# Kernel optimization log

Hardware: AMD Instinct MI355X
Metric: run time of the kernel (lower is better)

## Reference

```python
import jax, jax.numpy as jnp
import numpy as np

N_NODES = 100000
N_EDGES = 1600000
DIM = 64


def setup_inputs() -> dict:
    key = jax.random.key(0)
    ks = jax.random.split(key, 10)
    return {
        "h_real": jax.random.normal(ks[0], (N_NODES, DIM), dtype=jnp.float32),
        "h_imag": jax.random.normal(ks[1], (N_NODES, DIM), dtype=jnp.float32),
        "d": jax.random.uniform(ks[2], (N_NODES,), dtype=jnp.float32),
        "w_real": jax.random.normal(ks[3], (N_EDGES,), dtype=jnp.float32),
        "w_imag": jax.random.normal(ks[4], (N_EDGES,), dtype=jnp.float32),
        "src": jax.random.randint(ks[5], (N_EDGES,), 0, N_NODES, dtype=jnp.int32),
        "dst": jax.random.randint(ks[6], (N_EDGES,), 0, N_NODES, dtype=jnp.int32),
        "W1": jax.random.normal(ks[7], (DIM, DIM), dtype=jnp.float32) * (1.414 / np.sqrt(DIM)),
        "b1": jnp.zeros((DIM,), dtype=jnp.float32),
        "W2": jax.random.normal(ks[8], (DIM, DIM), dtype=jnp.float32) * (1.414 / np.sqrt(DIM)),
        "b2": jnp.zeros((DIM,), dtype=jnp.float32),
    }


def reference(h_real, h_imag, d, w_real, w_imag, src, dst, W1, b1, W2, b2):
    n = h_real.shape[0]
    # per-edge complex coefficient e = d_dst * d_src * (w_real + i w_imag)
    dd = d[dst] * d[src]                      # [E]
    e_r = (dd * w_real)[:, None]              # [E,1]
    e_i = (dd * w_imag)[:, None]              # [E,1]
    hr = h_real[src]                          # [E,D]
    hi = h_imag[src]                          # [E,D]
    # complex multiply e * h, fused single pass over edges
    m_r = e_r * hr - e_i * hi                 # [E,D]
    m_i = e_i * hr + e_r * hi                 # [E,D]
    z_real = jax.ops.segment_sum(m_r, dst, num_segments=n)  # [N,D]
    z_imag = jax.ops.segment_sum(m_i, dst, num_segments=n)  # [N,D]
    # note: original overwrites z_real first, then z_imag uses the NEW z_real
    zr = (z_real @ W1.T + b1) - (z_imag @ W2.T + b2)
    zi = (zr @ W2.T + b2) + (z_imag @ W1.T + b1)
    return zr, zi
```

## Files before the change

kernel.cpp:

```cpp
#include <hip/hip_runtime.h>
#include <hip/hip_bf16.h>

#define N_NODES 100000
#define N_EDGES 1600000
#define DIM 64

#define TILE 4096
#define B1 ((N_EDGES + TILE - 1) / TILE)
#define K1 ((N_NODES + 255) / 256)
#define NCOUNTS (K1 * B1)
#define SCAN_BLOCK 1024
#define NSB ((NCOUNTS + SCAN_BLOCK - 1) / SCAN_BLOCK)
#define PACKB ((N_NODES * DIM + 255) / 256)
#define PLACE_CAP 4736

typedef __attribute__((ext_vector_type(8))) short bf16x8;
typedef __attribute__((ext_vector_type(4))) float f32x4;

#if defined(__has_builtin)
#if __has_builtin(__builtin_amdgcn_fdot2_f32_bf16)
#define HAVE_DOT2 1
typedef __attribute__((ext_vector_type(2))) __bf16 bf16x2v;
#endif
#endif


__device__ __forceinline__ unsigned pack_bf16x2(float lo, float hi) {
  unsigned ulo = (unsigned)__hip_bfloat16_raw(__float2bfloat16(lo)).x;
  unsigned uhi = (unsigned)__hip_bfloat16_raw(__float2bfloat16(hi)).x;
  return ulo | (uhi << 16);
}
__device__ __forceinline__ float unpack_lo(unsigned u) {
  return __int_as_float((int)(u << 16));
}
__device__ __forceinline__ float unpack_hi(unsigned u) {
  return __int_as_float((int)(u & 0xFFFF0000u));
}
__device__ __forceinline__ unsigned short f2bf(float x) {
  return __hip_bfloat16_raw(__float2bfloat16(x)).x;
}

__global__ __launch_bounds__(256) void setup_fused_kernel(
    const float* __restrict__ h_real, const float* __restrict__ h_imag,
    unsigned* __restrict__ hpack, const float* __restrict__ W1,
    const float* __restrict__ b1, const float* __restrict__ W2,
    const float* __restrict__ b2, unsigned short* __restrict__ At,
    float* __restrict__ cvec, const int* __restrict__ dst,
    int* __restrict__ counts) {
  const int bid = blockIdx.x;
  const int tid = threadIdx.x;
  if (bid < PACKB) {
    const int i = bid * 256 + tid;
    if (i < N_NODES * DIM) hpack[i] = pack_bf16x2(h_real[i], h_imag[i]);
    return;
  }
  if (bid < PACKB + 64) {
    const int idx = (bid - PACKB) * 256 + tid;
    if (idx < 128 * 128) {
      const int n = idx >> 7, k = idx & 127;
      float v;
      if (n < 64) {
        v = (k < 64) ? W1[n * 64 + k] : -W2[n * 64 + (k - 64)];
      } else {
        const int nn = n - 64;
        if (k < 64) {
          float s = 0.0f;
          for (int j = 0; j < 64; ++j) s += W1[j * 64 + k] * W2[nn * 64 + j];
          v = s;
        } else {
          const int kk = k - 64;
          float s = 0.0f;
          for (int j = 0; j < 64; ++j) s += W2[j * 64 + kk] * W2[nn * 64 + j];
          v = W1[nn * 64 + kk] - s;
        }
      }
      At[n * 128 + k] = f2bf(v);
    }
    if (idx < 128) {
      if (idx < 64) {
        cvec[idx] = b1[idx] - b2[idx];
      } else {
        const int nn = idx - 64;
        float s = 0.0f;
        for (int j = 0; j < 64; ++j) s += (b1[j] - b2[j]) * W2[nn * 64 + j];
        cvec[idx] = s + b1[nn] + b2[nn];
      }
    }
    return;
  }
  __shared__ int lh[K1];
  const int hb = bid - PACKB - 64;
  for (int i = tid; i < K1; i += 256) lh[i] = 0;
  __syncthreads();
  const int e0 = hb * TILE;
  const int e1 = min(e0 + TILE, N_EDGES);
  for (int e = e0 + tid; e < e1; e += 256) atomicAdd(&lh[dst[e] >> 8], 1);
  __syncthreads();
  for (int b = tid; b < K1; b += 256) counts[b * B1 + hb] = lh[b];
}

__global__ __launch_bounds__(SCAN_BLOCK) void scan1_kernel(
    int* __restrict__ cnt, int* __restrict__ bsum) {
  __shared__ int s[SCAN_BLOCK];
  const int tid = threadIdx.x;
  const int i = blockIdx.x * SCAN_BLOCK + tid;
  const int v = (i < NCOUNTS) ? cnt[i] : 0;
  s[tid] = v;
  __syncthreads();
#pragma unroll
  for (int off = 1; off < SCAN_BLOCK; off <<= 1) {
    int t = (tid >= off) ? s[tid - off] : 0;
    __syncthreads();
    s[tid] += t;
    __syncthreads();
  }
  if (i < NCOUNTS) cnt[i] = s[tid] - v;
  if (tid == SCAN_BLOCK - 1) bsum[blockIdx.x] = s[tid];
}

__global__ void scan2_kernel(const int* __restrict__ bsum, int* __restrict__ bpre) {
  if (threadIdx.x == 0 && blockIdx.x == 0) {
    int run = 0;
    for (int b = 0; b < NSB; ++b) {
      bpre[b] = run;
      run += bsum[b];
    }
  }
}

__global__ __launch_bounds__(SCAN_BLOCK) void scan3_kernel(
    int* __restrict__ cnt, const int* __restrict__ bpre) {
  const int i = blockIdx.x * SCAN_BLOCK + threadIdx.x;
  if (i < NCOUNTS) cnt[i] += bpre[blockIdx.x];
}

__global__ __launch_bounds__(512) void partition_kernel(
    const int* __restrict__ src, const int* __restrict__ dst,
    const float* __restrict__ dvec,
    const float* __restrict__ w_real, const float* __restrict__ w_imag,
    const int* __restrict__ coffs, unsigned long long* __restrict__ records) {
  __shared__ unsigned long long stage[TILE];
  __shared__ unsigned short sb[TILE];
  __shared__ int lhist[512];
  __shared__ int lbase[K1];
  __shared__ int lcur[K1];
  __shared__ int gbase[K1];
  const int tid = threadIdx.x;
  const int blk = blockIdx.x;
  const int e0 = blk * TILE;
  const int cnt_t = min(TILE, N_EDGES - e0);

  lhist[tid] = 0;
  __syncthreads();
  for (int j = tid; j < cnt_t; j += 512) atomicAdd(&lhist[dst[e0 + j] >> 8], 1);
  __syncthreads();
  const int myc = lhist[tid];
  __syncthreads();
#pragma unroll
  for (int off = 1; off < 512; off <<= 1) {
    int v = (tid >= off) ? lhist[tid - off] : 0;
    __syncthreads();
    lhist[tid] += v;
    __syncthreads();
  }
  if (tid < K1) {
    const int ex = lhist[tid] - myc;
    lbase[tid] = ex;
    lcur[tid] = ex;
    gbase[tid] = coffs[tid * B1 + blk];
  }
  __syncthreads();

  for (int j = tid; j < cnt_t; j += 512) {
    const int e = e0 + j;
    const int t = dst[e];
    const int s = src[e];
    const int b = t >> 8;
    const float ds = dvec[s];
    const unsigned lo = (unsigned)s | ((unsigned)(t & 255) << 17);
    const unsigned hi = pack_bf16x2(ds * w_real[e], ds * w_imag[e]);
    const int r = atomicAdd(&lcur[b], 1);
    stage[r] = ((unsigned long long)hi << 32) | lo;
    sb[r] = (unsigned short)b;
  }
  __syncthreads();
  for (int i = tid; i < cnt_t; i += 512) {
    const int b = sb[i];
    records[gbase[b] + (i - lbase[b])] = stage[i];
  }
}

__global__ __launch_bounds__(256) void place_kernel(
    unsigned long long* __restrict__ records, const int* __restrict__ coffs,
    int* __restrict__ inc) {
  const int b = blockIdx.x;
  const int tid = threadIdx.x;
  const int bstart = coffs[b * B1];
  const int bend = (b == K1 - 1) ? N_EDGES : coffs[(b + 1) * B1];
  const int cnt = min(bend - bstart, PLACE_CAP);
  const int nbase = b << 8;
  const int nn = min(256, N_NODES - nbase);

  __shared__ unsigned long long stage[PLACE_CAP];
  __shared__ int ncnt[256];
  __shared__ int ncur[256];

  ncnt[tid] = 0;
  __syncthreads();
  for (int i = tid; i < cnt; i += 256) {
    const unsigned long long rec = records[bstart + i];
    stage[i] = rec;
    atomicAdd(&ncnt[((unsigned)rec >> 17) & 255], 1);
  }
  __syncthreads();
  const int myc = ncnt[tid];
  __syncthreads();
#pragma unroll
  for (int off = 1; off < 256; off <<= 1) {
    int v = (tid >= off) ? ncnt[tid - off] : 0;
    __syncthreads();
    ncnt[tid] += v;
    __syncthreads();
  }
  const int base = bstart + ncnt[tid] - myc;
  ncur[tid] = base;
  if (tid < nn) inc[nbase + tid] = base + myc;
  __syncthreads();
  for (int i = tid; i < cnt; i += 256) {
    const unsigned long long rec = stage[i];
    const int pos = atomicAdd(&ncur[((unsigned)rec >> 17) & 255], 1);
    records[pos] = rec;
  }
}

__global__ __launch_bounds__(1024) void pull_fused_kernel(
    const uint2* __restrict__ records, const int* __restrict__ inc,
    const float* __restrict__ dvec, const unsigned* __restrict__ hpack,
    const unsigned short* __restrict__ At, const float* __restrict__ cvec,
    float* __restrict__ zr_out, float* __restrict__ zi_out) {
  __shared__ __align__(16) unsigned short zs[16][136];
  const int lane = threadIdx.x & 63;
  const int wave = threadIdx.x >> 6;
  const int q4 = lane >> 4;
  const int m16 = lane & 15;
  const int node0 = blockIdx.x * 16;
  const int n = node0 + wave;

  const int start = (n == 0) ? 0 : inc[n - 1];
  const int end = inc[n];
  const int deg = end - start;
  const unsigned* __restrict__ hb = hpack + 4 * m16;

  float sr0 = 0.f, sr1 = 0.f, sr2 = 0.f, sr3 = 0.f;
  float si0 = 0.f, si1 = 0.f, si2 = 0.f, si3 = 0.f;

#if HAVE_DOT2
#define DOT2(acc, w, h)                                                     \
  acc = __builtin_amdgcn_fdot2_f32_bf16(__builtin_bit_cast(bf16x2v, (w)),   \
                                        __builtin_bit_cast(bf16x2v, (h)),   \
                                        acc, false)
#else
#define DOT2(acc, w, h)                                                     \
  {                                                                         \
    const float _wl = unpack_lo(w), _wh = unpack_hi(w);                     \
    const float _hl = unpack_lo(h), _hh = unpack_hi(h);                     \
    acc += _wl * _hl + _wh * _hh;                                           \
  }
#endif

#define ACC4(RR)                                                            \
  {                                                                         \
    const unsigned wneg = (RR).y ^ 0x80000000u;                             \
    const unsigned wswp = ((RR).y >> 16) | ((RR).y << 16);                  \
    const uint4 hv = *reinterpret_cast<const uint4*>(                       \
        hb + (size_t)((RR).x & 0x1FFFF) * DIM);                             \
    DOT2(sr0, wneg, hv.x); DOT2(si0, wswp, hv.x);                           \
    DOT2(sr1, wneg, hv.y); DOT2(si1, wswp, hv.y);                           \
    DOT2(sr2, wneg, hv.z); DOT2(si2, wswp, hv.z);                           \
    DOT2(sr3, wneg, hv.w); DOT2(si3, wswp, hv.w);                           \
  }

  int p = start + q4;
  const int nfull = deg >> 2;
  int i = 0;
  for (; i + 2 <= nfull; i += 2) {
    const uint2 r0 = records[p];
    const uint2 r1 = records[p + 4];
    ACC4(r0);
    ACC4(r1);
    p += 8;
  }
  if (i < nfull) {
    const uint2 r0 = records[p];
    ACC4(r0);
    p += 4;
  }
  if (p < end) {
    const uint2 r0 = records[p];
    ACC4(r0);
  }
#undef ACC4
#undef DOT2

#define QRED(v)                  \
  v += __shfl_xor(v, 16);        \
  v += __shfl_xor(v, 32);
  QRED(sr0) QRED(sr1) QRED(sr2) QRED(sr3)
  QRED(si0) QRED(si1) QRED(si2) QRED(si3)
#undef QRED

  const float dn = dvec[n];
  if (lane < 16) {
    uint2 rv, iv;
    rv.x = pack_bf16x2(dn * sr0, dn * sr1);
    rv.y = pack_bf16x2(dn * sr2, dn * sr3);
    iv.x = pack_bf16x2(dn * si0, dn * si1);
    iv.y = pack_bf16x2(dn * si2, dn * si3);
    *reinterpret_cast<uint2*>(&zs[wave][4 * lane]) = rv;
    *reinterpret_cast<uint2*>(&zs[wave][64 + 4 * lane]) = iv;
  }
  __syncthreads();

  if (wave < 8) {
    const int t = wave;
    const int m = lane & 15;
    const int q = lane >> 4;

    bf16x8 a[4];
#pragma unroll
    for (int c = 0; c < 4; ++c)
      a[c] = *reinterpret_cast<const bf16x8*>(&zs[m][c * 32 + q * 8]);

    f32x4 acc = (f32x4){0.f, 0.f, 0.f, 0.f};
    const unsigned short* brow = At + (size_t)(t * 16 + m) * 128 + q * 8;
#pragma unroll
    for (int c = 0; c < 4; ++c) {
      bf16x8 bfrag = *reinterpret_cast<const bf16x8*>(brow + c * 32);
      acc = __builtin_amdgcn_mfma_f32_16x16x32_bf16(a[c], bfrag, acc, 0, 0, 0);
    }

    const int nf = t * 16 + m;
    const float bias = cvec[nf];
    float* outp = (nf < 64) ? zr_out : zi_out;
    const int nn = nf & 63;
#pragma unroll
    for (int r = 0; r < 4; ++r) {
      const int node = node0 + q * 4 + r;
      outp[(size_t)node * 64 + nn] = acc[r] + bias;
    }
  }
}

extern "C" void kernel_launch(void* const* d_in, const int* in_sizes, int n_in,
                              void* d_out, int out_size, void* d_ws, size_t ws_size,
                              hipStream_t stream) {
  const float* h_real = (const float*)d_in[0];
  const float* h_imag = (const float*)d_in[1];
  const float* dvec   = (const float*)d_in[2];
  const float* w_real = (const float*)d_in[3];
  const float* w_imag = (const float*)d_in[4];
  const int*   src    = (const int*)d_in[5];
  const int*   dst    = (const int*)d_in[6];
  const float* W1     = (const float*)d_in[7];
  const float* b1     = (const float*)d_in[8];
  const float* W2     = (const float*)d_in[9];
  const float* b2     = (const float*)d_in[10];

  char* ws = (char*)d_ws;
  unsigned short* At = (unsigned short*)ws;
  float* cvec = (float*)(ws + 128 * 128 * 2);
  unsigned long long* records = (unsigned long long*)(ws + 33792);
  unsigned* hpack = (unsigned*)(ws + 33792 + (size_t)N_EDGES * 8);
  int* counts = (int*)(ws + 33792 + (size_t)N_EDGES * 8 + (size_t)N_NODES * DIM * 4);
  int* bsum = counts + NCOUNTS;
  int* bpre = bsum + NSB;
  int* inc  = bpre + NSB;

  float* zr_out = (float*)d_out;
  float* zi_out = zr_out + (size_t)N_NODES * DIM;

  setup_fused_kernel<<<PACKB + 64 + B1, 256, 0, stream>>>(
      h_real, h_imag, (unsigned*)hpack, W1, b1, W2, b2, At, cvec, dst, counts);
  scan1_kernel<<<NSB, SCAN_BLOCK, 0, stream>>>(counts, bsum);
  scan2_kernel<<<1, 64, 0, stream>>>(bsum, bpre);
  scan3_kernel<<<NSB, SCAN_BLOCK, 0, stream>>>(counts, bpre);
  partition_kernel<<<B1, 512, 0, stream>>>(src, dst, dvec, w_real, w_imag,
                                           counts, records);
  place_kernel<<<K1, 256, 0, stream>>>(records, counts, inc);
  pull_fused_kernel<<<N_NODES / 16, 1024, 0, stream>>>(
      (const uint2*)records, inc, dvec, hpack, At, cvec, zr_out, zi_out);
}
```

Measured before the change: 277.7 us.

## Balance pull work across block edges, use wave-shuffle scans, drop scan3, vectorize packing

The pull kernel now gives each 16-lane group an equal share of the block's edge range instead of one wave per node. Groups flush partial sums into a shared fp32 tile with LDS atomics whenever the destination node changes, and records and gathered rows are prefetched eight at a time. All block-level scans switch from LDS Hillis-Steele loops to wave shuffle scans. scan3 is removed by adding the block prefix at the consumer side, and the h packing is vectorized to float4. This targets load imbalance from the degree distribution and barrier-heavy scans, at the cost of LDS atomic traffic and a smaller 512-thread block.

```diff
diff --git a/kernel.cpp b/kernel.cpp
--- a/kernel.cpp
+++ b/kernel.cpp
@@ -11,7 +11,7 @@
 #define NCOUNTS (K1 * B1)
 #define SCAN_BLOCK 1024
 #define NSB ((NCOUNTS + SCAN_BLOCK - 1) / SCAN_BLOCK)
-#define PACKB ((N_NODES * DIM + 255) / 256)
+#define PACKB4 ((N_NODES * DIM / 4 + 255) / 256)
 #define PLACE_CAP 4736
 
 typedef __attribute__((ext_vector_type(8))) short bf16x8;
@@ -49,13 +49,20 @@
     int* __restrict__ counts) {
   const int bid = blockIdx.x;
   const int tid = threadIdx.x;
-  if (bid < PACKB) {
+  if (bid < PACKB4) {
     const int i = bid * 256 + tid;
-    if (i < N_NODES * DIM) hpack[i] = pack_bf16x2(h_real[i], h_imag[i]);
+    const float4 hr = ((const float4*)h_real)[i];
+    const float4 hi = ((const float4*)h_imag)[i];
+    uint4 o;
+    o.x = pack_bf16x2(hr.x, hi.x);
+    o.y = pack_bf16x2(hr.y, hi.y);
+    o.z = pack_bf16x2(hr.z, hi.z);
+    o.w = pack_bf16x2(hr.w, hi.w);
+    ((uint4*)hpack)[i] = o;
     return;
   }
-  if (bid < PACKB + 64) {
-    const int idx = (bid - PACKB) * 256 + tid;
+  if (bid < PACKB4 + 64) {
+    const int idx = (bid - PACKB4) * 256 + tid;
     if (idx < 128 * 128) {
       const int n = idx >> 7, k = idx & 127;
       float v;
@@ -89,7 +96,7 @@
     return;
   }
   __shared__ int lh[K1];
-  const int hb = bid - PACKB - 64;
+  const int hb = bid - PACKB4 - 64;
   for (int i = tid; i < K1; i += 256) lh[i] = 0;
   __syncthreads();
   const int e0 = hb * TILE;
@@ -101,51 +108,80 @@
 
 __global__ __launch_bounds__(SCAN_BLOCK) void scan1_kernel(
     int* __restrict__ cnt, int* __restrict__ bsum) {
-  __shared__ int s[SCAN_BLOCK];
-  const int tid = threadIdx.x;
+  __shared__ int wsum[16];
+  const int tid = threadIdx.x;
+  const int lane = tid & 63;
+  const int w = tid >> 6;
   const int i = blockIdx.x * SCAN_BLOCK + tid;
-  const int v = (i < NCOUNTS) ? cnt[i] : 0;
-  s[tid] = v;
-  __syncthreads();
-#pragma unroll
-  for (int off = 1; off < SCAN_BLOCK; off <<= 1) {
-    int t = (tid >= off) ? s[tid - off] : 0;
-    __syncthreads();
-    s[tid] += t;
-    __syncthreads();
-  }
-  if (i < NCOUNTS) cnt[i] = s[tid] - v;
-  if (tid == SCAN_BLOCK - 1) bsum[blockIdx.x] = s[tid];
-}
-
-__global__ void scan2_kernel(const int* __restrict__ bsum, int* __restrict__ bpre) {
-  if (threadIdx.x == 0 && blockIdx.x == 0) {
-    int run = 0;
-    for (int b = 0; b < NSB; ++b) {
-      bpre[b] = run;
-      run += bsum[b];
-    }
-  }
-}
-
-__global__ __launch_bounds__(SCAN_BLOCK) void scan3_kernel(
-    int* __restrict__ cnt, const int* __restrict__ bpre) {
-  const int i = blockIdx.x * SCAN_BLOCK + threadIdx.x;
-  if (i < NCOUNTS) cnt[i] += bpre[blockIdx.x];
+  const int orig = (i < NCOUNTS) ? cnt[i] : 0;
+  int v = orig;
+#pragma unroll
+  for (int off = 1; off < 64; off <<= 1) {
+    int t = __shfl_up(v, off);
+    if (lane >= off) v += t;
+  }
+  if (lane == 63) wsum[w] = v;
+  __syncthreads();
+  if (w == 0) {
+    int s = (lane < 16) ? wsum[lane] : 0;
+#pragma unroll
+    for (int off = 1; off < 16; off <<= 1) {
+      int t = __shfl_up(s, off);
+      if (lane >= off) s += t;
+    }
+    if (lane < 16) wsum[lane] = s;
+  }
+  __syncthreads();
+  const int wex = (w == 0) ? 0 : wsum[w - 1];
+  if (i < NCOUNTS) cnt[i] = wex + v - orig;
+  if (tid == SCAN_BLOCK - 1) bsum[blockIdx.x] = wex + v;
+}
+
+__global__ __launch_bounds__(256) void scan2_kernel(
+    const int* __restrict__ bsum, int* __restrict__ bpre) {
+  __shared__ int wsum[4];
+  const int tid = threadIdx.x;
+  const int lane = tid & 63;
+  const int w = tid >> 6;
+  const int orig = (tid < NSB) ? bsum[tid] : 0;
+  int v = orig;
+#pragma unroll
+  for (int off = 1; off < 64; off <<= 1) {
+    int t = __shfl_up(v, off);
+    if (lane >= off) v += t;
+  }
+  if (lane == 63) wsum[w] = v;
+  __syncthreads();
+  if (w == 0) {
+    int s = (lane < 4) ? wsum[lane] : 0;
+#pragma unroll
+    for (int off = 1; off < 4; off <<= 1) {
+      int t = __shfl_up(s, off);
+      if (lane >= off) s += t;
+    }
+    if (lane < 4) wsum[lane] = s;
+  }
+  __syncthreads();
+  const int wex = (w == 0) ? 0 : wsum[w - 1];
+  if (tid < NSB) bpre[tid] = wex + v - orig;
 }
 
 __global__ __launch_bounds__(512) void partition_kernel(
     const int* __restrict__ src, const int* __restrict__ dst,
     const float* __restrict__ dvec,
     const float* __restrict__ w_real, const float* __restrict__ w_imag,
-    const int* __restrict__ coffs, unsigned long long* __restrict__ records) {
+    const int* __restrict__ coffs, const int* __restrict__ bpre,
+    unsigned long long* __restrict__ records) {
   __shared__ unsigned long long stage[TILE];
   __shared__ unsigned short sb[TILE];
   __shared__ int lhist[512];
   __shared__ int lbase[K1];
   __shared__ int lcur[K1];
   __shared__ int gbase[K1];
-  const int tid = threadIdx.x;
+  __shared__ int wsum[8];
+  const int tid = threadIdx.x;
+  const int lane = tid & 63;
+  const int w = tid >> 6;
   const int blk = blockIdx.x;
   const int e0 = blk * TILE;
   const int cnt_t = min(TILE, N_EDGES - e0);
@@ -155,19 +191,30 @@
   for (int j = tid; j < cnt_t; j += 512) atomicAdd(&lhist[dst[e0 + j] >> 8], 1);
   __syncthreads();
   const int myc = lhist[tid];
-  __syncthreads();
-#pragma unroll
-  for (int off = 1; off < 512; off <<= 1) {
-    int v = (tid >= off) ? lhist[tid - off] : 0;
-    __syncthreads();
-    lhist[tid] += v;
-    __syncthreads();
-  }
+  int v = myc;
+#pragma unroll
+  for (int off = 1; off < 64; off <<= 1) {
+    int t = __shfl_up(v, off);
+    if (lane >= off) v += t;
+  }
+  if (lane == 63) wsum[w] = v;
+  __syncthreads();
+  if (w == 0) {
+    int s = (lane < 8) ? wsum[lane] : 0;
+#pragma unroll
+    for (int off = 1; off < 8; off <<= 1) {
+      int t = __shfl_up(s, off);
+      if (lane >= off) s += t;
+    }
+    if (lane < 8) wsum[lane] = s;
+  }
+  __syncthreads();
+  const int ex = v + ((w == 0) ? 0 : wsum[w - 1]) - myc;
   if (tid < K1) {
-    const int ex = lhist[tid] - myc;
     lbase[tid] = ex;
     lcur[tid] = ex;
-    gbase[tid] = coffs[tid * B1 + blk];
+    const int ci = tid * B1 + blk;
+    gbase[tid] = coffs[ci] + bpre[ci >> 10];
   }
   __syncthreads();
 
@@ -192,11 +239,20 @@
 
 __global__ __launch_bounds__(256) void place_kernel(
     unsigned long long* __restrict__ records, const int* __restrict__ coffs,
-    int* __restrict__ inc) {
+    const int* __restrict__ bpre, int* __restrict__ inc) {
   const int b = blockIdx.x;
   const int tid = threadIdx.x;
-  const int bstart = coffs[b * B1];
-  const int bend = (b == K1 - 1) ? N_EDGES : coffs[(b + 1) * B1];
+  const int lane = tid & 63;
+  const int w = tid >> 6;
+  const int ci0 = b * B1;
+  const int bstart = coffs[ci0] + bpre[ci0 >> 10];
+  int bend;
+  if (b == K1 - 1) {
+    bend = N_EDGES;
+  } else {
+    const int ci1 = (b + 1) * B1;
+    bend = coffs[ci1] + bpre[ci1 >> 10];
+  }
   const int cnt = min(bend - bstart, PLACE_CAP);
   const int nbase = b << 8;
   const int nn = min(256, N_NODES - nbase);
@@ -204,6 +260,7 @@
   __shared__ unsigned long long stage[PLACE_CAP];
   __shared__ int ncnt[256];
   __shared__ int ncur[256];
+  __shared__ int wsum[4];
 
   ncnt[tid] = 0;
   __syncthreads();
@@ -214,15 +271,26 @@
   }
   __syncthreads();
   const int myc = ncnt[tid];
-  __syncthreads();
-#pragma unroll
-  for (int off = 1; off < 256; off <<= 1) {
-    int v = (tid >= off) ? ncnt[tid - off] : 0;
-    __syncthreads();
-    ncnt[tid] += v;
-    __syncthreads();
-  }
-  const int base = bstart + ncnt[tid] - myc;
+  int v = myc;
+#pragma unroll
+  for (int off = 1; off < 64; off <<= 1) {
+    int t = __shfl_up(v, off);
+    if (lane >= off) v += t;
+  }
+  if (lane == 63) wsum[w] = v;
+  __syncthreads();
+  if (w == 0) {
+    int s = (lane < 4) ? wsum[lane] : 0;
+#pragma unroll
+    for (int off = 1; off < 4; off <<= 1) {
+      int t = __shfl_up(s, off);
+      if (lane >= off) s += t;
+    }
+    if (lane < 4) wsum[lane] = s;
+  }
+  __syncthreads();
+  const int incl = v + ((w == 0) ? 0 : wsum[w - 1]);
+  const int base = bstart + incl - myc;
   ncur[tid] = base;
   if (tid < nn) inc[nbase + tid] = base + myc;
   __syncthreads();
@@ -233,95 +301,129 @@
   }
 }
 
-__global__ __launch_bounds__(1024) void pull_fused_kernel(
+__global__ __launch_bounds__(512, 6) void pull_fused_kernel(
     const uint2* __restrict__ records, const int* __restrict__ inc,
     const float* __restrict__ dvec, const unsigned* __restrict__ hpack,
     const unsigned short* __restrict__ At, const float* __restrict__ cvec,
     float* __restrict__ zr_out, float* __restrict__ zi_out) {
+  __shared__ __align__(16) float zacc[16][128];
   __shared__ __align__(16) unsigned short zs[16][136];
-  const int lane = threadIdx.x & 63;
-  const int wave = threadIdx.x >> 6;
+  const int tid = threadIdx.x;
+  const int lane = tid & 63;
+  const int wave = tid >> 6;
   const int q4 = lane >> 4;
   const int m16 = lane & 15;
+  const int gq = (wave << 2) | q4;
   const int node0 = blockIdx.x * 16;
-  const int n = node0 + wave;
-
-  const int start = (n == 0) ? 0 : inc[n - 1];
-  const int end = inc[n];
-  const int deg = end - start;
+  const int nbl = node0 & 255;
+
+  ((f32x4*)zacc)[tid] = (f32x4){0.f, 0.f, 0.f, 0.f};
+  __syncthreads();
+
+  const int e0b = (node0 == 0) ? 0 : inc[node0 - 1];
+  const int e1b = inc[node0 + 15];
+  const int chunk = (e1b - e0b + 31) >> 5;
+  const int qs = e0b + gq * chunk;
+  const int qe = min(qs + chunk, e1b);
+
   const unsigned* __restrict__ hb = hpack + 4 * m16;
 
   float sr0 = 0.f, sr1 = 0.f, sr2 = 0.f, sr3 = 0.f;
   float si0 = 0.f, si1 = 0.f, si2 = 0.f, si3 = 0.f;
+  int cur = -1;
 
 #if HAVE_DOT2
-#define DOT2(acc, w, h)                                                     \
-  acc = __builtin_amdgcn_fdot2_f32_bf16(__builtin_bit_cast(bf16x2v, (w)),   \
-                                        __builtin_bit_cast(bf16x2v, (h)),   \
+#define DOT2(acc, w_, h_)                                                   \
+  acc = __builtin_amdgcn_fdot2_f32_bf16(__builtin_bit_cast(bf16x2v, (w_)),  \
+                                        __builtin_bit_cast(bf16x2v, (h_)),  \
                                         acc, false)
 #else
-#define DOT2(acc, w, h)                                                     \
+#define DOT2(acc, w_, h_)                                                   \
   {                                                                         \
-    const float _wl = unpack_lo(w), _wh = unpack_hi(w);                     \
-    const float _hl = unpack_lo(h), _hh = unpack_hi(h);                     \
+    const float _wl = unpack_lo(w_), _wh = unpack_hi(w_);                   \
+    const float _hl = unpack_lo(h_), _hh = unpack_hi(h_);                   \
     acc += _wl * _hl + _wh * _hh;                                           \
   }
 #endif
 
-#define ACC4(RR)                                                            \
+#define FLUSH_ACC()                                                         \
   {                                                                         \
-    const unsigned wneg = (RR).y ^ 0x80000000u;                             \
-    const unsigned wswp = ((RR).y >> 16) | ((RR).y << 16);                  \
-    const uint4 hv = *reinterpret_cast<const uint4*>(                       \
-        hb + (size_t)((RR).x & 0x1FFFF) * DIM);                             \
-    DOT2(sr0, wneg, hv.x); DOT2(si0, wswp, hv.x);                           \
-    DOT2(sr1, wneg, hv.y); DOT2(si1, wswp, hv.y);                           \
-    DOT2(sr2, wneg, hv.z); DOT2(si2, wswp, hv.z);                           \
-    DOT2(sr3, wneg, hv.w); DOT2(si3, wswp, hv.w);                           \
-  }
-
-  int p = start + q4;
-  const int nfull = deg >> 2;
-  int i = 0;
-  for (; i + 2 <= nfull; i += 2) {
-    const uint2 r0 = records[p];
-    const uint2 r1 = records[p + 4];
-    ACC4(r0);
-    ACC4(r1);
-    p += 8;
-  }
-  if (i < nfull) {
-    const uint2 r0 = records[p];
-    ACC4(r0);
-    p += 4;
-  }
-  if (p < end) {
-    const uint2 r0 = records[p];
-    ACC4(r0);
-  }
-#undef ACC4
+    float* zp = &zacc[cur][m16 * 4];                                        \
+    atomicAdd(zp + 0, sr0);                                                 \
+    atomicAdd(zp + 1, sr1);                                                 \
+    atomicAdd(zp + 2, sr2);                                                 \
+    atomicAdd(zp + 3, sr3);                                                 \
+    atomicAdd(zp + 64, si0);                                                \
+    atomicAdd(zp + 65, si1);                                                \
+    atomicAdd(zp + 66, si2);                                                \
+    atomicAdd(zp + 67, si3);                                                \
+  }
+
+#define STEP(RJ, HJ, JJ)                                                    \
+  {                                                                         \
+    const bool v_ = (base + JJ) < qe;                                       \
+    const int nl_ = v_ ? (int)(((RJ).x >> 17) & 255) - nbl : cur;           \
+    if (nl_ != cur) {                                                       \
+      if (cur >= 0) FLUSH_ACC();                                            \
+      sr0 = sr1 = sr2 = sr3 = si0 = si1 = si2 = si3 = 0.f;                  \
+      cur = nl_;                                                            \
+    }                                                                       \
+    if (v_) {                                                               \
+      const unsigned wneg = (RJ).y ^ 0x80000000u;                           \
+      const unsigned wswp = ((RJ).y >> 16) | ((RJ).y << 16);                \
+      DOT2(sr0, wneg, (HJ).x); DOT2(si0, wswp, (HJ).x);                     \
+      DOT2(sr1, wneg, (HJ).y); DOT2(si1, wswp, (HJ).y);                     \
+      DOT2(sr2, wneg, (HJ).z); DOT2(si2, wswp, (HJ).z);                     \
+      DOT2(sr3, wneg, (HJ).w); DOT2(si3, wswp, (HJ).w);                     \
+    }                                                                       \
+  }
+
+  for (int base = qs; base < qe; base += 8) {
+    const int lim = qe - 1;
+    const uint2 r0 = records[min(base + 0, lim)];
+    const uint2 r1 = records[min(base + 1, lim)];
+    const uint2 r2 = records[min(base + 2, lim)];
+    const uint2 r3 = records[min(base + 3, lim)];
+    const uint2 r4 = records[min(base + 4, lim)];
+    const uint2 r5 = records[min(base + 5, lim)];
+    const uint2 r6 = records[min(base + 6, lim)];
+    const uint2 r7 = records[min(base + 7, lim)];
+    const uint4 h0 = *reinterpret_cast<const uint4*>(hb + (size_t)(r0.x & 0x1FFFF) * DIM);
+    const uint4 h1 = *reinterpret_cast<const uint4*>(hb + (size_t)(r1.x & 0x1FFFF) * DIM);
+    const uint4 h2 = *reinterpret_cast<const uint4*>(hb + (size_t)(r2.x & 0x1FFFF) * DIM);
+    const uint4 h3 = *reinterpret_cast<const uint4*>(hb + (size_t)(r3.x & 0x1FFFF) * DIM);
+    const uint4 h4 = *reinterpret_cast<const uint4*>(hb + (size_t)(r4.x & 0x1FFFF) * DIM);
+    const uint4 h5 = *reinterpret_cast<const uint4*>(hb + (size_t)(r5.x & 0x1FFFF) * DIM);
+    const uint4 h6 = *reinterpret_cast<const uint4*>(hb + (size_t)(r6.x & 0x1FFFF) * DIM);
+    const uint4 h7 = *reinterpret_cast<const uint4*>(hb + (size_t)(r7.x & 0x1FFFF) * DIM);
+    STEP(r0, h0, 0)
+    STEP(r1, h1, 1)
+    STEP(r2, h2, 2)
+    STEP(r3, h3, 3)
+    STEP(r4, h4, 4)
+    STEP(r5, h5, 5)
+    STEP(r6, h6, 6)
+    STEP(r7, h7, 7)
+  }
+  if (cur >= 0) FLUSH_ACC();
+#undef STEP
+#undef FLUSH_ACC
 #undef DOT2
-
-#define QRED(v)                  \
-  v += __shfl_xor(v, 16);        \
-  v += __shfl_xor(v, 32);
-  QRED(sr0) QRED(sr1) QRED(sr2) QRED(sr3)
-  QRED(si0) QRED(si1) QRED(si2) QRED(si3)
-#undef QRED
-
-  const float dn = dvec[n];
-  if (lane < 16) {
-    uint2 rv, iv;
-    rv.x = pack_bf16x2(dn * sr0, dn * sr1);
-    rv.y = pack_bf16x2(dn * sr2, dn * sr3);
-    iv.x = pack_bf16x2(dn * si0, dn * si1);
-    iv.y = pack_bf16x2(dn * si2, dn * si3);
-    *reinterpret_cast<uint2*>(&zs[wave][4 * lane]) = rv;
-    *reinterpret_cast<uint2*>(&zs[wave][64 + 4 * lane]) = iv;
-  }
-  __syncthreads();
-
-  if (wave < 8) {
+  __syncthreads();
+
+  {
+    const int idx0 = tid * 4;
+    const int nd = idx0 >> 7;
+    const int dd = idx0 & 127;
+    const float dn = dvec[node0 + nd];
+    uint2 pk;
+    pk.x = pack_bf16x2(zacc[nd][dd] * dn, zacc[nd][dd + 1] * dn);
+    pk.y = pack_bf16x2(zacc[nd][dd + 2] * dn, zacc[nd][dd + 3] * dn);
+    *reinterpret_cast<uint2*>(&zs[nd][dd]) = pk;
+  }
+  __syncthreads();
+
+  {
     const int t = wave;
     const int m = lane & 15;
     const int q = lane >> 4;
@@ -342,11 +444,11 @@
     const int nf = t * 16 + m;
     const float bias = cvec[nf];
     float* outp = (nf < 64) ? zr_out : zi_out;
-    const int nn = nf & 63;
+    const int nnn = nf & 63;
 #pragma unroll
     for (int r = 0; r < 4; ++r) {
       const int node = node0 + q * 4 + r;
-      outp[(size_t)node * 64 + nn] = acc[r] + bias;
+      outp[(size_t)node * 64 + nnn] = acc[r] + bias;
     }
   }
 }
@@ -379,14 +481,13 @@
   float* zr_out = (float*)d_out;
   float* zi_out = zr_out + (size_t)N_NODES * DIM;
 
-  setup_fused_kernel<<<PACKB + 64 + B1, 256, 0, stream>>>(
+  setup_fused_kernel<<<PACKB4 + 64 + B1, 256, 0, stream>>>(
       h_real, h_imag, (unsigned*)hpack, W1, b1, W2, b2, At, cvec, dst, counts);
   scan1_kernel<<<NSB, SCAN_BLOCK, 0, stream>>>(counts, bsum);
-  scan2_kernel<<<1, 64, 0, stream>>>(bsum, bpre);
-  scan3_kernel<<<NSB, SCAN_BLOCK, 0, stream>>>(counts, bpre);
+  scan2_kernel<<<1, 256, 0, stream>>>(bsum, bpre);
   partition_kernel<<<B1, 512, 0, stream>>>(src, dst, dvec, w_real, w_imag,
-                                           counts, records);
-  place_kernel<<<K1, 256, 0, stream>>>(records, counts, inc);
-  pull_fused_kernel<<<N_NODES / 16, 1024, 0, stream>>>(
+                                           counts, bpre, records);
+  place_kernel<<<K1, 256, 0, stream>>>(records, counts, bpre, inc);
+  pull_fused_kernel<<<N_NODES / 16, 512, 0, stream>>>(
       (const uint2*)records, inc, dvec, hpack, At, cvec, zr_out, zi_out);
 }
```

Result: slower. 378.7 us (+36.4%).
